# Kernel tuning notes

Hardware: AMD Instinct MI355X
Metric: run time of the kernel (lower is better)

The kernel has to match this reference:

```python
import jax, jax.numpy as jnp
import numpy as np

B, S, D = 4, 2048, 1024


def setup_inputs() -> dict:
    key = jax.random.key(0)
    k1, k2, k3, k4 = jax.random.split(key, 4)
    scale = 1.0 / np.sqrt(D)
    return {
        "X_emb": jax.random.normal(k1, (B, S, D), dtype=jnp.float32),
        "W_q": jax.random.normal(k2, (D, D), dtype=jnp.float32) * scale,
        "W_k": jax.random.normal(k3, (D, D), dtype=jnp.float32) * scale,
        "W_v": jax.random.normal(k4, (D, D), dtype=jnp.float32) * scale,
    }


def reference(X_emb, W_q, W_k, W_v):
    # nn.Linear(bias=False): x @ W.T
    Xq = jnp.einsum('bsd,ed->bse', X_emb, W_q)
    Xk = jnp.einsum('bsd,ed->bse', X_emb, W_k)
    Xv = jnp.einsum('bsd,ed->bse', X_emb, W_v)
    S_len = X_emb.shape[-2]
    # scores [B, S, S]; causal mask (strict upper triangle -> -inf)
    att = jnp.einsum('bqe,bke->bqk', Xq, Xk)
    causal = jnp.tril(jnp.ones((S_len, S_len), dtype=bool))
    att = jnp.where(causal, att, -jnp.inf)
    # note: original masks before scaling; -inf / sqrt(d) is still -inf
    att = att / jnp.sqrt(jnp.asarray(Xk.shape[-1], att.dtype))
    w = jax.nn.softmax(att, axis=-1)
    return jnp.einsum('bqk,bke->bqe', w, Xv)
```

## Files before the change

kernel.cpp:

```cpp
#include <hip/hip_runtime.h>
#include <stdint.h>
#include <math.h>

typedef __attribute__((ext_vector_type(8))) __bf16 bf16x8;
typedef __attribute__((ext_vector_type(4))) float f32x4;

__device__ __forceinline__ unsigned short f2bf(float f) {
    unsigned u = __float_as_uint(f);
    u += 0x7FFF + ((u >> 16) & 1);
    return (unsigned short)(u >> 16);
}
__device__ __forceinline__ float bf2f(unsigned short u) {
    return __uint_as_float((unsigned)u << 16);
}

__global__ __launch_bounds__(256)
void convert_all_k(const float* __restrict__ X, const float* __restrict__ Wq,
                   const float* __restrict__ Wk, const float* __restrict__ Wv,
                   unsigned short* __restrict__ Xb, unsigned short* __restrict__ Wb,
                   int n4x, int n4w) {
    const float* src;
    unsigned short* dst;
    int n4;
    if (blockIdx.y == 0) { src = X; dst = Xb; n4 = n4x; }
    else {
        src = blockIdx.y == 1 ? Wq : (blockIdx.y == 2 ? Wk : Wv);
        dst = Wb + (size_t)(blockIdx.y - 1) * n4w * 4;
        n4 = n4w;
    }
    int i = blockIdx.x * blockDim.x + threadIdx.x;
    int stride = gridDim.x * blockDim.x;
    for (; i < n4; i += stride) {
        float4 v = reinterpret_cast<const float4*>(src)[i];
        ushort4 o;
        o.x = f2bf(v.x); o.y = f2bf(v.y); o.z = f2bf(v.z); o.w = f2bf(v.w);
        reinterpret_cast<ushort4*>(dst)[i] = o;
    }
}

__device__ __forceinline__ void gload16(const unsigned short* g, unsigned short* l) {
    __builtin_amdgcn_global_load_lds(
        (const __attribute__((address_space(1))) unsigned int*)g,
        (__attribute__((address_space(3))) unsigned int*)l, 16, 0, 0);
}

template <typename CT, int MODE>
__global__ __launch_bounds__(256, 2)
void gemm8(const unsigned short* __restrict__ A, const unsigned short* __restrict__ B,
           CT* __restrict__ C, int lda, int ldb, int ldc, int K,
           long long sA, long long sB, long long sC, float scale, int totj)
{
    constexpr int BM = 128, BN = 128;
    constexpr int FM = 4, FN = 4;

    const int nbx = gridDim.x;
    const int nwg = nbx * gridDim.y;
    const int orig = blockIdx.y * nbx + blockIdx.x;
    const int q8 = nwg >> 3, r8 = nwg & 7;
    const int xcd = orig & 7, idx = orig >> 3;
    const int work = (xcd < r8 ? xcd * (q8 + 1) : r8 * (q8 + 1) + (xcd - r8) * q8) + idx;

    A += (long long)blockIdx.z * sA;
    B += (long long)blockIdx.z * sB;
    C += (long long)blockIdx.z * sC;

    __shared__ unsigned short As[2][BM * 64];
    __shared__ unsigned short Bs[2][BN * 64];

    const int t    = threadIdx.x;
    const int lane = t & 63;
    const int wid  = t >> 6;
    const int wm   = wid >> 1, wn = wid & 1;
    const int rsel = lane & 15;
    const int gsel = lane >> 4;
    const int srow = t >> 3;
    const int swz  = ((t & 7) ^ (srow & 7)) * 8;

    auto run_tile = [&](int br, int bc, int kmax, bool first) {
        const int m0 = br * BM, n0 = bc * BN;
        f32x4 acc[FM][FN];
#pragma unroll
        for (int m = 0; m < FM; ++m)
#pragma unroll
            for (int n = 0; n < FN; ++n) acc[m][n] = (f32x4){0.f, 0.f, 0.f, 0.f};

        const unsigned short* gpA[4];
        const unsigned short* gpB[4];
#pragma unroll
        for (int i = 0; i < 4; ++i) {
            gpA[i] = A + (long long)(m0 + srow + 32 * i) * lda + swz;
            gpB[i] = B + (long long)(n0 + srow + 32 * i) * ldb + swz;
        }

        auto stage = [&](int buf) {
#pragma unroll
            for (int i = 0; i < 4; ++i)
                gload16(gpA[i], &As[buf][i * 2048 + t * 8]);
#pragma unroll
            for (int i = 0; i < 4; ++i)
                gload16(gpB[i], &Bs[buf][i * 2048 + t * 8]);
#pragma unroll
            for (int i = 0; i < 4; ++i) { gpA[i] += 64; gpB[i] += 64; }
        };

        const int nk = kmax >> 6;
        if (!first) {
            __builtin_amdgcn_s_barrier();
            __builtin_amdgcn_sched_barrier(0);
        }
        stage(0);

        for (int kt = 0; kt < nk; ++kt) {
            const int c = kt & 1;
            __builtin_amdgcn_s_barrier();
            __builtin_amdgcn_sched_barrier(0);
            if (kt + 1 < nk) {
                stage(c ^ 1);
                asm volatile("s_waitcnt vmcnt(8)" ::: "memory");
            } else {
                asm volatile("s_waitcnt vmcnt(0)" ::: "memory");
            }
            __builtin_amdgcn_s_barrier();
            __builtin_amdgcn_sched_barrier(0);

            bf16x8 aF[FM][2], bF[FN][2];
#pragma unroll
            for (int m = 0; m < FM; ++m)
#pragma unroll
                for (int ks = 0; ks < 2; ++ks) {
                    int r  = wm * (FM * 16) + m * 16 + rsel;
                    int cc = ks * 4 + gsel;
                    aF[m][ks] = *reinterpret_cast<const bf16x8*>(
                        &As[c][r * 64 + ((cc ^ (r & 7)) * 8)]);
                }
#pragma unroll
            for (int n = 0; n < FN; ++n)
#pragma unroll
                for (int ks = 0; ks < 2; ++ks) {
                    int rb = wn * (FN * 16) + n * 16 + rsel;
                    int cc = ks * 4 + gsel;
                    bF[n][ks] = *reinterpret_cast<const bf16x8*>(
                        &Bs[c][rb * 64 + ((cc ^ (rb & 7)) * 8)]);
                }

            __builtin_amdgcn_s_setprio(1);
#pragma unroll
            for (int m = 0; m < FM; ++m)
#pragma unroll
                for (int n = 0; n < FN; ++n)
#pragma unroll
                    for (int ks = 0; ks < 2; ++ks)
                        acc[m][n] = __builtin_amdgcn_mfma_f32_16x16x32_bf16(
                            aF[m][ks], bF[n][ks], acc[m][n], 0, 0, 0);
            __builtin_amdgcn_s_setprio(0);
        }

        const int rowl = gsel * 4;
#pragma unroll
        for (int m = 0; m < FM; ++m) {
#pragma unroll
            for (int n = 0; n < FN; ++n) {
#pragma unroll
                for (int i = 0; i < 4; ++i) {
                    int r  = m0 + wm * (FM * 16) + m * 16 + rowl + i;
                    int cI = n0 + wn * (FN * 16) + n * 16 + rsel;
                    float v = acc[m][n][i] * scale;
                    if constexpr (sizeof(CT) == 2)
                        ((unsigned short*)C)[(long long)r * ldc + cI] = f2bf(v);
                    else
                        ((float*)C)[(long long)r * ldc + cI] = v;
                }
            }
        }
    };

    auto tri = [&](int w, int& br, int& bc) {
        int rr = (int)((sqrtf(8.0f * (float)w + 1.0f) - 1.0f) * 0.5f);
        while ((rr + 1) * (rr + 2) / 2 <= w) ++rr;
        while (rr * (rr + 1) / 2 > w) --rr;
        br = rr; bc = w - rr * (rr + 1) / 2;
    };

    if constexpr (MODE == 0) {
        run_tile(work / nbx, work % nbx, K, true);
    } else if constexpr (MODE == 1) {
        int br, bc;
        tri(work, br, bc);
        run_tile(br, bc, K, true);
        const int e = work >> 4;
        if ((work & 15) == 8 && nwg + e < totj) {
            tri(nwg + e, br, bc);
            run_tile(br, bc, K, false);
        }
    } else {
        const int chunk = work >> 4;
        const int lo    = work & 15;
        const int col   = work & 7;
        const int row   = (lo < 8) ? chunk : 15 - chunk;
        run_tile(row, col, (row + 1) * BM, true);
    }
}

__device__ __forceinline__ float waveMax(float v) {
#pragma unroll
    for (int o = 32; o > 0; o >>= 1) v = fmaxf(v, __shfl_xor(v, o, 64));
    return v;
}
__device__ __forceinline__ float waveSum(float v) {
#pragma unroll
    for (int o = 32; o > 0; o >>= 1) v += __shfl_xor(v, o, 64);
    return v;
}

__global__ __launch_bounds__(256)
void softmax_causal(const unsigned short* __restrict__ S, unsigned short* __restrict__ P,
                    int Slen) {
    __shared__ float e[2048];
    __shared__ float red[4];
    long long row = blockIdx.x;
    int q = (int)(row % Slen);
    const unsigned short* srow = S + row * (long long)Slen;
    unsigned short* prow = P + row * (long long)Slen;
    int len = q + 1;
    int t = threadIdx.x;

    int n8 = len >> 3;
    float mx = -3.0e38f;
    for (int i = t; i < n8; i += 256) {
        uint4 v = reinterpret_cast<const uint4*>(srow)[i];
        float f0 = __uint_as_float(v.x << 16), f1 = __uint_as_float(v.x & 0xffff0000u);
        float f2 = __uint_as_float(v.y << 16), f3 = __uint_as_float(v.y & 0xffff0000u);
        float f4 = __uint_as_float(v.z << 16), f5 = __uint_as_float(v.z & 0xffff0000u);
        float f6 = __uint_as_float(v.w << 16), f7 = __uint_as_float(v.w & 0xffff0000u);
        e[8 * i + 0] = f0; e[8 * i + 1] = f1; e[8 * i + 2] = f2; e[8 * i + 3] = f3;
        e[8 * i + 4] = f4; e[8 * i + 5] = f5; e[8 * i + 6] = f6; e[8 * i + 7] = f7;
        mx = fmaxf(mx, fmaxf(fmaxf(fmaxf(f0, f1), fmaxf(f2, f3)),
                             fmaxf(fmaxf(f4, f5), fmaxf(f6, f7))));
    }
    if (t < (len & 7)) {
        float v = bf2f(srow[n8 * 8 + t]);
        e[n8 * 8 + t] = v;
        mx = fmaxf(mx, v);
    }
    mx = waveMax(mx);
    if ((t & 63) == 0) red[t >> 6] = mx;
    __syncthreads();
    mx = fmaxf(fmaxf(red[0], red[1]), fmaxf(red[2], red[3]));

    float sum = 0.f;
    for (int k = t; k < len; k += 256) {
        float v = __expf(e[k] - mx);
        e[k] = v;
        sum += v;
    }
    sum = waveSum(sum);
    __syncthreads();
    if ((t & 63) == 0) red[t >> 6] = sum;
    __syncthreads();
    sum = red[0] + red[1] + red[2] + red[3];
    float inv = 1.0f / sum;

    int wlim = ((q >> 7) + 1) << 7;
    __syncthreads();
    for (int i = t; i < (wlim >> 2); i += 256) {
        int k = 4 * i;
        ushort4 o;
        o.x = (k + 0 < len) ? f2bf(e[k + 0] * inv) : (unsigned short)0;
        o.y = (k + 1 < len) ? f2bf(e[k + 1] * inv) : (unsigned short)0;
        o.z = (k + 2 < len) ? f2bf(e[k + 2] * inv) : (unsigned short)0;
        o.w = (k + 3 < len) ? f2bf(e[k + 3] * inv) : (unsigned short)0;
        reinterpret_cast<ushort4*>(prow)[i] = o;
    }
}

extern "C" void kernel_launch(void* const* d_in, const int* in_sizes, int n_in,
                              void* d_out, int out_size, void* d_ws, size_t ws_size,
                              hipStream_t stream) {
    const int B = 4, S = 2048, D = 1024;
    const float* X  = (const float*)d_in[0];
    const float* Wq = (const float*)d_in[1];
    const float* Wk = (const float*)d_in[2];
    const float* Wv = (const float*)d_in[3];
    float* out = (float*)d_out;

    char* ws = (char*)d_ws;
    unsigned short* Xb  = (unsigned short*)ws; ws += (size_t)B * S * D * 2;
    unsigned short* Wqb = (unsigned short*)ws; ws += (size_t)D * D * 2;
    unsigned short* Wkb = (unsigned short*)ws; ws += (size_t)D * D * 2;
    unsigned short* Wvb = (unsigned short*)ws; ws += (size_t)D * D * 2;
    unsigned short* Qb  = (unsigned short*)ws; ws += (size_t)B * S * D * 2;
    unsigned short* Kb  = (unsigned short*)ws; ws += (size_t)B * S * D * 2;
    unsigned short* Vt  = (unsigned short*)ws; ws += (size_t)B * S * D * 2;
    unsigned short* Sc  = (unsigned short*)ws; ws += (size_t)B * S * S * 2;
    unsigned short* P   = (unsigned short*)ws; ws += (size_t)B * S * S * 2;

    convert_all_k<<<dim3(2048, 4), 256, 0, stream>>>(
        X, Wq, Wk, Wv, Xb, Wqb, B * S * D / 4, D * D / 4);

    dim3 blk(256);
    gemm8<unsigned short, 0><<<dim3(D / 128, B * S / 128, 2), blk, 0, stream>>>(
        Xb, Wqb, Qb, D, D, D, D, 0, (long long)D * D, (long long)B * S * D, 1.0f, 0);

    gemm8<unsigned short, 0><<<dim3(S / 128, D / 128, B), blk, 0, stream>>>(
        Wvb, Xb, Vt, D, D, S, D, 0, (long long)S * D, (long long)D * S, 1.0f, 0);

    gemm8<unsigned short, 1><<<dim3(8, 16, B), blk, 0, stream>>>(
        Qb, Kb, Sc, D, D, S, D, (long long)S * D, (long long)S * D, (long long)S * S,
        0.03125f, 136);

    softmax_causal<<<B * S, 256, 0, stream>>>(Sc, P, S);

    gemm8<float, 3><<<dim3(8, 16, B), blk, 0, stream>>>(
        P, Vt, out, S, S, D, S, (long long)S * S, (long long)D * S, (long long)S * D,
        1.0f, 0);
}
```

Before: 173.0 us.

## Reassociate attention: fold Wq^T Wk into one matrix and apply Wv after PV

Scores are computed as X·(Wq^T Wk)·X^T by precomputing the DxD product M with a split-K GEMM plus a reduce kernel, then multiplying X by M once. This replaces the separate Q and K projections. The value projection is moved after the attention product, P·X then ·Wv^T, using a transposed bf16 copy of X produced by a new tiled transpose/convert kernel. FLOPs drop slightly, but it adds an extra bf16 rounding of the intermediate products and more kernel launches.

```diff
diff --git a/kernel.cpp b/kernel.cpp
--- a/kernel.cpp
+++ b/kernel.cpp
@@ -15,26 +15,73 @@
 }
 
 __global__ __launch_bounds__(256)
-void convert_all_k(const float* __restrict__ X, const float* __restrict__ Wq,
-                   const float* __restrict__ Wk, const float* __restrict__ Wv,
-                   unsigned short* __restrict__ Xb, unsigned short* __restrict__ Wb,
-                   int n4x, int n4w) {
+void convt_k(const float* __restrict__ X, const float* __restrict__ Wq,
+             const float* __restrict__ Wk, const float* __restrict__ Wv,
+             unsigned short* __restrict__ Xb, unsigned short* __restrict__ XbT,
+             unsigned short* __restrict__ WqT, unsigned short* __restrict__ WkT,
+             unsigned short* __restrict__ Wvb) {
+    const int S = 2048, D = 1024;
+    const int z = blockIdx.z;
     const float* src;
-    unsigned short* dst;
-    int n4;
-    if (blockIdx.y == 0) { src = X; dst = Xb; n4 = n4x; }
-    else {
-        src = blockIdx.y == 1 ? Wq : (blockIdx.y == 2 ? Wk : Wv);
-        dst = Wb + (size_t)(blockIdx.y - 1) * n4w * 4;
-        n4 = n4w;
-    }
+    unsigned short* dstP = nullptr;
+    unsigned short* dstT = nullptr;
+    int rows;
+    if (z < 4)      { src = X + (size_t)z * S * D; dstP = Xb + (size_t)z * S * D;
+                      dstT = XbT + (size_t)z * D * S; rows = S; }
+    else if (z == 4){ src = Wq; dstT = WqT; rows = D; }
+    else if (z == 5){ src = Wk; dstT = WkT; rows = D; }
+    else            { src = Wv; dstP = Wvb; rows = D; }
+    const int r0 = blockIdx.y * 64, c0 = blockIdx.x * 64;
+    if (r0 >= rows) return;
+
+    __shared__ float tile[64][65];
+    const int t = threadIdx.x;
+    const int tr = t >> 4;
+    const int tc4 = t & 15;
+#pragma unroll
+    for (int p = 0; p < 4; ++p) {
+        int r = p * 16 + tr;
+        float4 v = *reinterpret_cast<const float4*>(&src[(size_t)(r0 + r) * 1024 + c0 + tc4 * 4]);
+        if (dstP) {
+            ushort4 o; o.x = f2bf(v.x); o.y = f2bf(v.y); o.z = f2bf(v.z); o.w = f2bf(v.w);
+            *reinterpret_cast<ushort4*>(&dstP[(size_t)(r0 + r) * 1024 + c0 + tc4 * 4]) = o;
+        }
+        if (dstT) {
+            tile[r][tc4 * 4 + 0] = v.x; tile[r][tc4 * 4 + 1] = v.y;
+            tile[r][tc4 * 4 + 2] = v.z; tile[r][tc4 * 4 + 3] = v.w;
+        }
+    }
+    if (!dstT) return;
+    __syncthreads();
+    const int ldT = rows;
+#pragma unroll
+    for (int p = 0; p < 4; ++p) {
+        int c = p * 16 + tr;
+        ushort4 o;
+        o.x = f2bf(tile[tc4 * 4 + 0][c]);
+        o.y = f2bf(tile[tc4 * 4 + 1][c]);
+        o.z = f2bf(tile[tc4 * 4 + 2][c]);
+        o.w = f2bf(tile[tc4 * 4 + 3][c]);
+        *reinterpret_cast<ushort4*>(&dstT[(size_t)(c0 + c) * ldT + r0 + tc4 * 4]) = o;
+    }
+}
+
+__global__ __launch_bounds__(256)
+void reduce4_k(const float* __restrict__ p, unsigned short* __restrict__ o, int n4) {
+    const int slab = 1024 * 1024 / 4;
     int i = blockIdx.x * blockDim.x + threadIdx.x;
     int stride = gridDim.x * blockDim.x;
     for (; i < n4; i += stride) {
-        float4 v = reinterpret_cast<const float4*>(src)[i];
-        ushort4 o;
-        o.x = f2bf(v.x); o.y = f2bf(v.y); o.z = f2bf(v.z); o.w = f2bf(v.w);
-        reinterpret_cast<ushort4*>(dst)[i] = o;
+        float4 a = reinterpret_cast<const float4*>(p)[i];
+        float4 b = reinterpret_cast<const float4*>(p)[i + slab];
+        float4 c = reinterpret_cast<const float4*>(p)[i + 2 * slab];
+        float4 d = reinterpret_cast<const float4*>(p)[i + 3 * slab];
+        ushort4 u;
+        u.x = f2bf(a.x + b.x + c.x + d.x);
+        u.y = f2bf(a.y + b.y + c.y + d.y);
+        u.z = f2bf(a.z + b.z + c.z + d.z);
+        u.w = f2bf(a.w + b.w + c.w + d.w);
+        reinterpret_cast<ushort4*>(o)[i] = u;
     }
 }
 
@@ -284,33 +331,38 @@
     float* out = (float*)d_out;
 
     char* ws = (char*)d_ws;
-    unsigned short* Xb  = (unsigned short*)ws; ws += (size_t)B * S * D * 2;
-    unsigned short* Wqb = (unsigned short*)ws; ws += (size_t)D * D * 2;
-    unsigned short* Wkb = (unsigned short*)ws; ws += (size_t)D * D * 2;
-    unsigned short* Wvb = (unsigned short*)ws; ws += (size_t)D * D * 2;
-    unsigned short* Qb  = (unsigned short*)ws; ws += (size_t)B * S * D * 2;
-    unsigned short* Kb  = (unsigned short*)ws; ws += (size_t)B * S * D * 2;
-    unsigned short* Vt  = (unsigned short*)ws; ws += (size_t)B * S * D * 2;
-    unsigned short* Sc  = (unsigned short*)ws; ws += (size_t)B * S * S * 2;
-    unsigned short* P   = (unsigned short*)ws; ws += (size_t)B * S * S * 2;
-
-    convert_all_k<<<dim3(2048, 4), 256, 0, stream>>>(
-        X, Wq, Wk, Wv, Xb, Wqb, B * S * D / 4, D * D / 4);
+    unsigned short* Xb    = (unsigned short*)ws; ws += (size_t)B * S * D * 2;
+    unsigned short* XbT   = (unsigned short*)ws; ws += (size_t)B * D * S * 2;
+    unsigned short* WqT   = (unsigned short*)ws; ws += (size_t)D * D * 2;
+    unsigned short* WkT   = (unsigned short*)ws; ws += (size_t)D * D * 2;
+    unsigned short* Wvb   = (unsigned short*)ws; ws += (size_t)D * D * 2;
+    unsigned short* MTb   = (unsigned short*)ws; ws += (size_t)D * D * 2;
+    unsigned short* XMb   = (unsigned short*)ws; ws += (size_t)B * S * D * 2;
+    unsigned short* PXb   = (unsigned short*)ws; ws += (size_t)B * S * D * 2;
+    unsigned short* Sc    = (unsigned short*)ws; ws += (size_t)B * S * S * 2;
+    unsigned short* P     = (unsigned short*)ws; ws += (size_t)B * S * S * 2;
+    float*          Mpart = (float*)ws;          ws += (size_t)4 * D * D * 4;
+
+    convt_k<<<dim3(16, 32, 7), 256, 0, stream>>>(X, Wq, Wk, Wv, Xb, XbT, WqT, WkT, Wvb);
 
     dim3 blk(256);
-    gemm8<unsigned short, 0><<<dim3(D / 128, B * S / 128, 2), blk, 0, stream>>>(
-        Xb, Wqb, Qb, D, D, D, D, 0, (long long)D * D, (long long)B * S * D, 1.0f, 0);
-
-    gemm8<unsigned short, 0><<<dim3(S / 128, D / 128, B), blk, 0, stream>>>(
-        Wvb, Xb, Vt, D, D, S, D, 0, (long long)S * D, (long long)D * S, 1.0f, 0);
+    gemm8<float, 0><<<dim3(8, 8, 4), blk, 0, stream>>>(
+        WkT, WqT, Mpart, D, D, D, 256, 256, 256, (long long)D * D, 1.0f, 0);
+    reduce4_k<<<1024, 256, 0, stream>>>(Mpart, MTb, D * D / 4);
+
+    gemm8<unsigned short, 0><<<dim3(8, 64, 1), blk, 0, stream>>>(
+        Xb, MTb, XMb, D, D, D, D, 0, 0, 0, 1.0f, 0);
 
     gemm8<unsigned short, 1><<<dim3(8, 16, B), blk, 0, stream>>>(
-        Qb, Kb, Sc, D, D, S, D, (long long)S * D, (long long)S * D, (long long)S * S,
+        XMb, Xb, Sc, D, D, S, D, (long long)S * D, (long long)S * D, (long long)S * S,
         0.03125f, 136);
 
     softmax_causal<<<B * S, 256, 0, stream>>>(Sc, P, S);
 
-    gemm8<float, 3><<<dim3(8, 16, B), blk, 0, stream>>>(
-        P, Vt, out, S, S, D, S, (long long)S * S, (long long)D * S, (long long)S * D,
+    gemm8<unsigned short, 3><<<dim3(8, 16, B), blk, 0, stream>>>(
+        P, XbT, PXb, S, S, D, S, (long long)S * S, (long long)D * S, (long long)S * D,
         1.0f, 0);
-}
+
+    gemm8<float, 0><<<dim3(8, 64, 1), blk, 0, stream>>>(
+        PXb, Wvb, out, D, D, D, D, 0, 0, 0, 1.0f, 0);
+}
```

Measured after the change: 169.5 us. -2.0%, faster.
